# Kernel tuning notes

Hardware: AMD Instinct MI355X
Metric: run time of the kernel (lower is better)

The kernel has to match this reference:

```python
import jax, jax.numpy as jnp
import numpy as np

B, N, M = 4, 512, 8192
QUERY_DIM, INPUT_DIM = 512, 256
HEADS, DIM_HEAD = 8, 64
ATT_DIM = HEADS * DIM_HEAD  # 512


def setup_inputs() -> dict:
    key = jax.random.key(0)
    ks = jax.random.split(key, 6)
    x = jax.random.normal(ks[0], (B, N, QUERY_DIM), dtype=jnp.float32)
    context = jax.random.normal(ks[1], (B, M, INPUT_DIM), dtype=jnp.float32)
    # Linear weights stored as [in, out] for x @ W
    Wq = jax.random.normal(ks[2], (QUERY_DIM, ATT_DIM), dtype=jnp.float32) / np.sqrt(QUERY_DIM)
    Wkv = jax.random.normal(ks[3], (INPUT_DIM, 2 * ATT_DIM), dtype=jnp.float32) / np.sqrt(INPUT_DIM)
    Wo = jax.random.normal(ks[4], (ATT_DIM, QUERY_DIM), dtype=jnp.float32) / np.sqrt(ATT_DIM)
    bo = jax.random.normal(ks[5], (QUERY_DIM,), dtype=jnp.float32) * 0.01
    return {"x": x, "context": context, "Wq": Wq, "Wkv": Wkv, "Wo": Wo, "bo": bo}


def reference(x, context, Wq, Wkv, Wo, bo):
    scale = DIM_HEAD ** -0.5
    q = x @ Wq                      # [B, N, H*D]
    kv = context @ Wkv              # [B, M, 2*H*D]
    k, v = jnp.split(kv, 2, axis=-1)
    # split heads: b n (h d) -> b h n d
    q = q.reshape(B, N, HEADS, DIM_HEAD).transpose(0, 2, 1, 3)
    k = k.reshape(B, M, HEADS, DIM_HEAD).transpose(0, 2, 1, 3)
    v = v.reshape(B, M, HEADS, DIM_HEAD).transpose(0, 2, 1, 3)
    scores = jnp.einsum('bhid,bhjd->bhij', q, k) * scale  # [B, H, N, M]
    attn = jax.nn.softmax(scores, axis=-1)
    out = jnp.einsum('bhij,bhjd->bhid', attn, v)           # [B, H, N, D]
    out = out.transpose(0, 2, 1, 3).reshape(B, N, ATT_DIM)
    return out @ Wo + bo
```

## Files before the change

kernel.cpp:

```cpp
#include <hip/hip_runtime.h>
#include <hip/hip_bf16.h>
#include <cstdint>

#define NB 4
#define NQ 512
#define NM 8192
#define NH 8
#define DH 64

typedef short bf16x8s __attribute__((ext_vector_type(8)));
typedef short bf16x4s __attribute__((ext_vector_type(4)));
typedef float f32x4  __attribute__((ext_vector_type(4)));

static __device__ __forceinline__ short f2bs(float f) {
    unsigned u = __builtin_bit_cast(unsigned, f);
    return (short)(unsigned short)((u + 0x8000u) >> 16);
}
static __device__ __forceinline__ unsigned pk2(float a, float b) {
    unsigned au = __builtin_bit_cast(unsigned, a) + 0x8000u;
    unsigned bu = __builtin_bit_cast(unsigned, b) + 0x8000u;
    return __builtin_amdgcn_perm(bu, au, 0x07060302u);
}

#if __has_builtin(__builtin_amdgcn_exp2f)
static __device__ __forceinline__ float fexp2(float x) { return __builtin_amdgcn_exp2f(x); }
#else
static __device__ __forceinline__ float fexp2(float x) { return exp2f(x); }
#endif

__global__ __launch_bounds__(256) void prep_weights(
    const float* __restrict__ Wq, const float* __restrict__ Wo,
    const float* __restrict__ Wkv,
    short* __restrict__ Wqf, short* __restrict__ Wof, short* __restrict__ Wkvf)
{
    const int t = threadIdx.x;
    const int w = t >> 6, ln = t & 63;
    const int m16 = ln & 15, quad = ln >> 4;
    int f = blockIdx.x * 4 + w;
    const float* src; short* dst; int N, KS, n0, ks;
    if (f < 512)       { src = Wq;  dst = Wqf;  N = 512;  KS = 16; n0 = f >> 4; ks = f & 15; }
    else if (f < 1024) { f -= 512;  src = Wo;  dst = Wof;  N = 512;  KS = 16; n0 = f >> 4; ks = f & 15; }
    else               { f -= 1024; src = Wkv; dst = Wkvf; N = 1024; KS = 8;  n0 = f >> 3; ks = f & 7; }
    const float* sp = src + (size_t)(ks * 32 + quad * 8) * N + n0 * 16 + m16;
    float v[8];
    #pragma unroll
    for (int j = 0; j < 8; ++j) v[j] = sp[(size_t)j * N];
    uint4 pkv = { pk2(v[0],v[1]), pk2(v[2],v[3]), pk2(v[4],v[5]), pk2(v[6],v[7]) };
    *(uint4*)(dst + ((size_t)(n0 * KS + ks) * 64 + ln) * 8) = pkv;
}

__device__ __forceinline__ void proj32_body(
    const float* __restrict__ A, const short* __restrict__ Wf,
    float* __restrict__ C, const float* __restrict__ bias,
    int tm, int tn, char* smemraw)
{
    short* As = (short*)smemraw;

    const int t = threadIdx.x;
    const int w = t >> 6, ln = t & 63;
    const int m16 = ln & 15, quad = ln >> 4;
    const int wm = w >> 1, wn = w & 1;

    const int ar = t >> 3, ac = (t & 7) << 3;

    const float* Ap = A + (size_t)(tm * 32 + ar) * 512 + ac;

    f32x4 acc[2] = {};

    {
        float4 a0 = *(const float4*)(Ap);
        float4 a1 = *(const float4*)(Ap + 4);
        uint4 wa = { pk2(a0.x,a0.y), pk2(a0.z,a0.w), pk2(a1.x,a1.y), pk2(a1.z,a1.w) };
        *(uint4*)&As[ar * 72 + ac] = wa;
    }

    #pragma unroll
    for (int k0 = 0; k0 < 512; k0 += 64) {
        short* Ab = As + ((k0 >> 6) & 1) * 2304;
        __syncthreads();

        bf16x8s bfr[2][2];
        #pragma unroll
        for (int ks = 0; ks < 2; ++ks)
            #pragma unroll
            for (int nt = 0; nt < 2; ++nt)
                bfr[ks][nt] = *(const bf16x8s*)(Wf +
                    ((size_t)((tn * 4 + wn * 2 + nt) * 16 + (k0 >> 5) + ks) * 64 + ln) * 8);

        bf16x8s afr[2];
        #pragma unroll
        for (int ks = 0; ks < 2; ++ks)
            afr[ks] = *(const bf16x8s*)&Ab[(wm * 16 + m16) * 72 + ks * 32 + quad * 8];

        float4 a0n, a1n;
        if (k0 + 64 < 512) {
            a0n = *(const float4*)(Ap + k0 + 64);
            a1n = *(const float4*)(Ap + k0 + 68);
        }

        #pragma unroll
        for (int ks = 0; ks < 2; ++ks)
            #pragma unroll
            for (int nt = 0; nt < 2; ++nt)
                acc[nt] = __builtin_amdgcn_mfma_f32_16x16x32_bf16(afr[ks], bfr[ks][nt], acc[nt], 0, 0, 0);

        if (k0 + 64 < 512) {
            short* Abn = As + ((((k0 >> 6) + 1) & 1)) * 2304;
            uint4 wa = { pk2(a0n.x,a0n.y), pk2(a0n.z,a0n.w), pk2(a1n.x,a1n.y), pk2(a1n.z,a1n.w) };
            *(uint4*)&Abn[ar * 72 + ac] = wa;
        }
    }

    const int row0 = tm * 32 + wm * 16 + quad * 4;
    const int col0 = tn * 64 + wn * 32;
    #pragma unroll
    for (int nt = 0; nt < 2; ++nt) {
        const int col = col0 + nt * 16 + m16;
        const float bb = bias ? bias[col] : 0.f;
        #pragma unroll
        for (int r = 0; r < 4; ++r)
            C[(size_t)(row0 + r) * 512 + col] = acc[nt][r] + bb;
    }
}

__device__ __forceinline__ void kv_body(
    const float* __restrict__ A, const short* __restrict__ Wkvf,
    short* __restrict__ Kf, short* __restrict__ Vf,
    int kvid, char* smemraw)
{
    short* As = (short*)smemraw;

    const int t  = threadIdx.x;
    const int tm = ((kvid >> 6) << 3) | (kvid & 7);
    const int tn = (kvid >> 3) & 7;
    const int w  = t >> 6, ln = t & 63;
    const int m16 = ln & 15, quad = ln >> 4;
    const int wm = w & 1, wn = w >> 1;

    const int ar = t >> 3;
    const int ac = (t & 7) << 2;

    const float* Abase = A + (size_t)(tm * 128 + ar) * 256 + ac;

    f32x4 acc[4][4] = {};

    {
        float4 av[4];
        #pragma unroll
        for (int p = 0; p < 4; ++p)
            av[p] = *(const float4*)(Abase + (size_t)p * 32 * 256);
        #pragma unroll
        for (int p = 0; p < 4; ++p) {
            uint2 wv = { pk2(av[p].x, av[p].y), pk2(av[p].z, av[p].w) };
            *(uint2*)&As[(p * 32 + ar) * 40 + ac] = wv;
        }
    }

    #pragma unroll
    for (int k0 = 0; k0 < 256; k0 += 32) {
        short* Ab = As + ((k0 >> 5) & 1) * 5120;
        __syncthreads();

        bf16x8s bfr[4];
        #pragma unroll
        for (int j = 0; j < 4; ++j)
            bfr[j] = *(const bf16x8s*)(Wkvf +
                ((size_t)((tn * 8 + wn * 4 + j) * 8 + (k0 >> 5)) * 64 + ln) * 8);

        bf16x8s af[4];
        #pragma unroll
        for (int i = 0; i < 4; ++i)
            af[i] = *(const bf16x8s*)&Ab[(wm * 64 + i * 16 + m16) * 40 + quad * 8];

        float4 avn[4];
        if (k0 + 32 < 256) {
            #pragma unroll
            for (int p = 0; p < 4; ++p)
                avn[p] = *(const float4*)(Abase + (size_t)p * 32 * 256 + k0 + 32);
        }

        #pragma unroll
        for (int i = 0; i < 4; ++i)
            #pragma unroll
            for (int j = 0; j < 4; ++j)
                acc[i][j] = __builtin_amdgcn_mfma_f32_16x16x32_bf16(af[i], bfr[j], acc[i][j], 0, 0, 0);

        if (k0 + 32 < 256) {
            short* Abn = As + (((k0 >> 5) + 1) & 1) * 5120;
            #pragma unroll
            for (int p = 0; p < 4; ++p) {
                uint2 wv = { pk2(avn[p].x, avn[p].y), pk2(avn[p].z, avn[p].w) };
                *(uint2*)&Abn[(p * 32 + ar) * 40 + ac] = wv;
            }
        }
    }

    const int col0 = tn * 128 + wn * 64;
    const int row0 = tm * 128 + wm * 64;
    const int b    = row0 >> 13;
    const int mr0  = row0 & (NM - 1);

    if (col0 < 512) {
        const int h = col0 >> 6;
        short* Kp = Kf + (size_t)(b * NH + h) * (NM * DH);
        #pragma unroll
        for (int i = 0; i < 4; ++i)
            #pragma unroll
            for (int j = 0; j < 4; ++j) {
                const int d = j * 16 + m16;
                #pragma unroll
                for (int r = 0; r < 4; ++r) {
                    const int key = mr0 + i * 16 + quad * 4 + r;
                    const int idx = ((key >> 4) * 2 + (d >> 5)) * 512
                                  + (((d >> 3) & 3) * 16 + (key & 15)) * 8 + (d & 7);
                    Kp[idx] = f2bs(acc[i][j][r]);
                }
            }
    } else {
        const int h = (col0 - 512) >> 6;
        short* Vp = Vf + (size_t)(b * NH + h) * (NM * DH);
        #pragma unroll
        for (int j = 0; j < 4; ++j)
            #pragma unroll
            for (int p = 0; p < 2; ++p) {
                uint4 v;
                v.x = pk2(acc[2*p    ][j][0], acc[2*p    ][j][1]);
                v.y = pk2(acc[2*p    ][j][2], acc[2*p    ][j][3]);
                v.z = pk2(acc[2*p + 1][j][0], acc[2*p + 1][j][1]);
                v.w = pk2(acc[2*p + 1][j][2], acc[2*p + 1][j][3]);
                *(uint4*)(Vp + ((size_t)(j * 256 + (mr0 >> 5) + p) * 64 + ln) * 8) = v;
            }
    }
}

__global__ __launch_bounds__(256) void gemm_kvq(
    const float* __restrict__ x,   const short* __restrict__ Wqf, float* __restrict__ q,
    const float* __restrict__ ctx, const short* __restrict__ Wkvf,
    short* __restrict__ Kf, short* __restrict__ Vf)
{
    __shared__ __align__(16) char smem[20480];
    if (blockIdx.x < 512)
        proj32_body(x, Wqf, q, nullptr, (int)(blockIdx.x >> 3), (int)(blockIdx.x & 7), smem);
    else
        kv_body(ctx, Wkvf, Kf, Vf, (int)(blockIdx.x - 512), smem);
}

__global__ __launch_bounds__(256) void gemm_proj32(
    const float* __restrict__ A, const short* __restrict__ Wf,
    float* __restrict__ C, const float* __restrict__ bias)
{
    __shared__ __align__(16) char smem[32 * 72 * 2 * 2];
    proj32_body(A, Wf, C, bias, (int)(blockIdx.x >> 3), (int)(blockIdx.x & 7), smem);
}

__global__ __launch_bounds__(512, 2) void attn_mfma(
    const float* __restrict__ Q,
    const short* __restrict__ Kfr,
    const short* __restrict__ Vfr,
    float* __restrict__ Og)
{
    __shared__ __align__(16) float Ob[2][64 * 66];
    __shared__ float lbuf[8 * 64];

    const int bid = blockIdx.x;
    const int xcd = bid & 7, g = bid >> 3;
    const int bh  = xcd * 4 + (g & 3);
    const int qt  = g >> 2;
    const int b   = bh >> 3, h = bh & 7;
    const int t   = threadIdx.x;
    const int w   = t >> 6, ln = t & 63;
    const int m16 = ln & 15, quad = ln >> 4;

    const short* Kbase = Kfr + (size_t)bh * (NM * DH);
    const short* Vbase = Vfr + (size_t)bh * (NM * DH);

    const float qsc = 0.125f * 1.44269504f;
    bf16x8s qf[4][2];
    #pragma unroll
    for (int mt = 0; mt < 4; ++mt) {
        const float* qrow = Q + ((size_t)(b * NQ + qt * 64 + mt * 16 + m16)) * 512 + h * 64;
        #pragma unroll
        for (int ks = 0; ks < 2; ++ks) {
            float4 x0 = *(const float4*)(qrow + ks * 32 + quad * 8);
            float4 x1 = *(const float4*)(qrow + ks * 32 + quad * 8 + 4);
            uint4 pkv = { pk2(x0.x * qsc, x0.y * qsc), pk2(x0.z * qsc, x0.w * qsc),
                          pk2(x1.x * qsc, x1.y * qsc), pk2(x1.z * qsc, x1.w * qsc) };
            qf[mt][ks] = *reinterpret_cast<bf16x8s*>(&pkv);
        }
    }

    bf16x4s ones4;
    #pragma unroll
    for (int j = 0; j < 4; ++j) ones4[j] = (short)0x3F80;

    f32x4 o[4][4] = {};
    f32x4 lsum[4] = {};

    bf16x8s kf[4][2];
    {
        const int kc = w * 64;
        #pragma unroll
        for (int nt = 0; nt < 4; ++nt)
            #pragma unroll
            for (int ks = 0; ks < 2; ++ks)
                kf[nt][ks] = *(const bf16x8s*)(Kbase + ((((kc >> 4) + nt) * 2 + ks) << 9) + ln * 8);
    }

    for (int it = 0; it < 16; ++it) {
        const int kc = it * 512 + w * 64;

        uint4 vraw[4][2];
        #pragma unroll
        for (int dt = 0; dt < 4; ++dt)
            #pragma unroll
            for (int kp = 0; kp < 2; ++kp)
                vraw[dt][kp] = *(const uint4*)(Vbase + ((size_t)(dt * 256 + (kc >> 5) + kp) * 64 + ln) * 8);

        f32x4 st[4][4] = {};
        #pragma unroll
        for (int kt = 0; kt < 4; ++kt)
            #pragma unroll
            for (int mt = 0; mt < 4; ++mt) {
                st[mt][kt] = __builtin_amdgcn_mfma_f32_16x16x32_bf16(kf[kt][0], qf[mt][0], st[mt][kt], 0, 0, 0);
                st[mt][kt] = __builtin_amdgcn_mfma_f32_16x16x32_bf16(kf[kt][1], qf[mt][1], st[mt][kt], 0, 0, 0);
            }

        if (it + 1 < 16) {
            const int kn = (it + 1) * 512 + w * 64;
            #pragma unroll
            for (int nt = 0; nt < 4; ++nt)
                #pragma unroll
                for (int ks = 0; ks < 2; ++ks)
                    kf[nt][ks] = *(const bf16x8s*)(Kbase + ((((kn >> 4) + nt) * 2 + ks) << 9) + ln * 8);
        }

        #pragma unroll
        for (int mt = 0; mt < 4; ++mt)
            #pragma unroll
            for (int kt = 0; kt < 4; ++kt) {
                const float p0 = fexp2(st[mt][kt][0]);
                const float p1 = fexp2(st[mt][kt][1]);
                const float p2 = fexp2(st[mt][kt][2]);
                const float p3 = fexp2(st[mt][kt][3]);
                uint2 pu = { pk2(p0, p1), pk2(p2, p3) };
                bf16x4s pbv = *reinterpret_cast<bf16x4s*>(&pu);
                const int kp = kt >> 1, hh = kt & 1;
                #pragma unroll
                for (int dt = 0; dt < 4; ++dt) {
                    uint2 vh = hh ? make_uint2(vraw[dt][kp].z, vraw[dt][kp].w)
                                  : make_uint2(vraw[dt][kp].x, vraw[dt][kp].y);
                    bf16x4s va = *reinterpret_cast<bf16x4s*>(&vh);
                    o[mt][dt] = __builtin_amdgcn_mfma_f32_16x16x16bf16_1k(va, pbv, o[mt][dt], 0, 0, 0);
                }
                lsum[mt] = __builtin_amdgcn_mfma_f32_16x16x16bf16_1k(ones4, pbv, lsum[mt], 0, 0, 0);
            }
    }

    if (quad == 0) {
        #pragma unroll
        for (int mt = 0; mt < 4; ++mt)
            lbuf[w * 64 + mt * 16 + m16] = lsum[mt][0];
    }
    if (w < 2) {
        float* dst = Ob[w];
        #pragma unroll
        for (int mt = 0; mt < 4; ++mt)
            #pragma unroll
            for (int dt = 0; dt < 4; ++dt)
                *(f32x4*)&dst[(mt * 16 + m16) * 66 + dt * 16 + quad * 4] = o[mt][dt];
    }
    __syncthreads();
    #pragma unroll
    for (int ph = 1; ph < 4; ++ph) {
        if ((w >> 1) == ph) {
            float* dst = Ob[w & 1];
            #pragma unroll
            for (int mt = 0; mt < 4; ++mt)
                #pragma unroll
                for (int dt = 0; dt < 4; ++dt) {
                    float* p = &dst[(mt * 16 + m16) * 66 + dt * 16 + quad * 4];
                    f32x4 cur = *(f32x4*)p;
                    cur += o[mt][dt];
                    *(f32x4*)p = cur;
                }
        }
        __syncthreads();
    }
    {
        const int row = t >> 3;
        const int d0  = (t & 7) << 3;
        float l = 0.f;
        #pragma unroll
        for (int wi = 0; wi < 8; ++wi) l += lbuf[wi * 64 + row];
        const float inv = 1.0f / l;
        float* op = Og + ((size_t)(b * NQ + qt * 64 + row)) * 512 + h * 64 + d0;
        #pragma unroll
        for (int j = 0; j < 2; ++j) {
            const int c = row * 66 + d0 + j * 4;
            float4 r;
            r.x = (Ob[0][c + 0] + Ob[1][c + 0]) * inv;
            r.y = (Ob[0][c + 1] + Ob[1][c + 1]) * inv;
            r.z = (Ob[0][c + 2] + Ob[1][c + 2]) * inv;
            r.w = (Ob[0][c + 3] + Ob[1][c + 3]) * inv;
            *(float4*)(op + j * 4) = r;
        }
    }
}

extern "C" void kernel_launch(void* const* d_in, const int* in_sizes, int n_in,
                              void* d_out, int out_size, void* d_ws, size_t ws_size,
                              hipStream_t stream) {
    (void)in_sizes; (void)n_in; (void)out_size; (void)ws_size;

    const float* x   = (const float*)d_in[0];
    const float* ctx = (const float*)d_in[1];
    const float* Wq  = (const float*)d_in[2];
    const float* Wkv = (const float*)d_in[3];
    const float* Wo  = (const float*)d_in[4];
    const float* bo  = (const float*)d_in[5];
    float* out = (float*)d_out;

    float* ws    = (float*)d_ws;
    float* q     = ws;
    float* attno = q + (size_t)2048 * 512;
    short* Kf    = (short*)(attno + (size_t)2048 * 512);
    short* Vf    = Kf + (size_t)NB * NH * NM * DH;
    short* Wqf   = Vf + (size_t)NB * NH * NM * DH;
    short* Wof   = Wqf + (size_t)512 * 512;
    short* Wkvf  = Wof + (size_t)512 * 512;

    prep_weights<<<dim3(384), dim3(256), 0, stream>>>(Wq, Wo, Wkv, Wqf, Wof, Wkvf);

    gemm_kvq<<<dim3(2560), dim3(256), 0, stream>>>(x, Wqf, q, ctx, Wkvf, Kf, Vf);

    attn_mfma<<<dim3(256), dim3(512), 0, stream>>>(q, Kf, Vf, attno);

    gemm_proj32<<<dim3(512), dim3(256), 0, stream>>>(attno, Wof, out, bo);
}
```

Baseline: 187.5 us.

## Split attention over key halves, merge in output projection, restructure KV GEMM

Attention now splits the key range into two halves per block (512 blocks instead of 256), writing unnormalized partial outputs and row sums. The output projection adds the two partials and normalizes them before the bf16 GEMM. The KV projection uses 512-thread blocks covering 256 output columns, stages weights through double-buffered LDS, and writes K via an LDS transpose for coalesced stores. MFMA sections get s_setprio hints. The aim is higher occupancy and parallelism, at the cost of an extra partial buffer and more LDS per block.

```diff
diff --git a/kernel.cpp b/kernel.cpp
--- a/kernel.cpp
+++ b/kernel.cpp
@@ -52,11 +52,10 @@
 __device__ __forceinline__ void proj32_body(
     const float* __restrict__ A, const short* __restrict__ Wf,
     float* __restrict__ C, const float* __restrict__ bias,
-    int tm, int tn, char* smemraw)
+    int tm, int tn, char* smemraw, int t)
 {
     short* As = (short*)smemraw;
 
-    const int t = threadIdx.x;
     const int w = t >> 6, ln = t & 63;
     const int m16 = ln & 15, quad = ln >> 4;
     const int wm = w >> 1, wn = w & 1;
@@ -123,99 +122,203 @@
     }
 }
 
+__device__ __forceinline__ void projo_body(
+    const float* __restrict__ A0, const float* __restrict__ A1,
+    const float* __restrict__ l0p, const float* __restrict__ l1p,
+    const short* __restrict__ Wf,
+    float* __restrict__ C, const float* __restrict__ bias,
+    int tm, int tn, char* smemraw, int t)
+{
+    short* As = (short*)smemraw;
+
+    const int w = t >> 6, ln = t & 63;
+    const int m16 = ln & 15, quad = ln >> 4;
+    const int wm = w >> 1, wn = w & 1;
+
+    const int ar = t >> 3, ac = (t & 7) << 3;
+
+    const int row = tm * 32 + ar;
+    const int lbase = ((row >> 9) * NH) * NQ + (row & 511);
+
+    float sc[8];
+    #pragma unroll
+    for (int h = 0; h < 8; ++h)
+        sc[h] = 1.0f / (l0p[lbase + h * NQ] + l1p[lbase + h * NQ]);
+
+    const float* Ap0 = A0 + (size_t)row * 512 + ac;
+    const float* Ap1 = A1 + (size_t)row * 512 + ac;
+
+    f32x4 acc[2] = {};
+
+    {
+        float4 a0 = *(const float4*)(Ap0);
+        float4 b0 = *(const float4*)(Ap1);
+        float4 a1 = *(const float4*)(Ap0 + 4);
+        float4 b1 = *(const float4*)(Ap1 + 4);
+        const float s = sc[0];
+        uint4 wa = { pk2((a0.x+b0.x)*s,(a0.y+b0.y)*s), pk2((a0.z+b0.z)*s,(a0.w+b0.w)*s),
+                     pk2((a1.x+b1.x)*s,(a1.y+b1.y)*s), pk2((a1.z+b1.z)*s,(a1.w+b1.w)*s) };
+        *(uint4*)&As[ar * 72 + ac] = wa;
+    }
+
+    #pragma unroll
+    for (int k0 = 0; k0 < 512; k0 += 64) {
+        short* Ab = As + ((k0 >> 6) & 1) * 2304;
+        __syncthreads();
+
+        bf16x8s bfr[2][2];
+        #pragma unroll
+        for (int ks = 0; ks < 2; ++ks)
+            #pragma unroll
+            for (int nt = 0; nt < 2; ++nt)
+                bfr[ks][nt] = *(const bf16x8s*)(Wf +
+                    ((size_t)((tn * 4 + wn * 2 + nt) * 16 + (k0 >> 5) + ks) * 64 + ln) * 8);
+
+        bf16x8s afr[2];
+        #pragma unroll
+        for (int ks = 0; ks < 2; ++ks)
+            afr[ks] = *(const bf16x8s*)&Ab[(wm * 16 + m16) * 72 + ks * 32 + quad * 8];
+
+        float4 a0n, b0n, a1n, b1n;
+        if (k0 + 64 < 512) {
+            a0n = *(const float4*)(Ap0 + k0 + 64);
+            b0n = *(const float4*)(Ap1 + k0 + 64);
+            a1n = *(const float4*)(Ap0 + k0 + 68);
+            b1n = *(const float4*)(Ap1 + k0 + 68);
+        }
+
+        #pragma unroll
+        for (int ks = 0; ks < 2; ++ks)
+            #pragma unroll
+            for (int nt = 0; nt < 2; ++nt)
+                acc[nt] = __builtin_amdgcn_mfma_f32_16x16x32_bf16(afr[ks], bfr[ks][nt], acc[nt], 0, 0, 0);
+
+        if (k0 + 64 < 512) {
+            short* Abn = As + ((((k0 >> 6) + 1) & 1)) * 2304;
+            const float s = sc[(k0 >> 6) + 1];
+            uint4 wa = { pk2((a0n.x+b0n.x)*s,(a0n.y+b0n.y)*s), pk2((a0n.z+b0n.z)*s,(a0n.w+b0n.w)*s),
+                         pk2((a1n.x+b1n.x)*s,(a1n.y+b1n.y)*s), pk2((a1n.z+b1n.z)*s,(a1n.w+b1n.w)*s) };
+            *(uint4*)&Abn[ar * 72 + ac] = wa;
+        }
+    }
+
+    const int row0 = tm * 32 + wm * 16 + quad * 4;
+    const int col0 = tn * 64 + wn * 32;
+    #pragma unroll
+    for (int nt = 0; nt < 2; ++nt) {
+        const int col = col0 + nt * 16 + m16;
+        const float bb = bias[col];
+        #pragma unroll
+        for (int r = 0; r < 4; ++r)
+            C[(size_t)(row0 + r) * 512 + col] = acc[nt][r] + bb;
+    }
+}
+
 __device__ __forceinline__ void kv_body(
     const float* __restrict__ A, const short* __restrict__ Wkvf,
     short* __restrict__ Kf, short* __restrict__ Vf,
     int kvid, char* smemraw)
 {
     short* As = (short*)smemraw;
+    short* Ws = (short*)(smemraw + 20480);
 
     const int t  = threadIdx.x;
-    const int tm = ((kvid >> 6) << 3) | (kvid & 7);
-    const int tn = (kvid >> 3) & 7;
+    const int tm  = ((kvid >> 5) << 3) | (kvid & 7);
+    const int tn0 = (kvid >> 3) & 3;
     const int w  = t >> 6, ln = t & 63;
     const int m16 = ln & 15, quad = ln >> 4;
     const int wm = w & 1, wn = w >> 1;
 
-    const int ar = t >> 3;
-    const int ac = (t & 7) << 2;
-
-    const float* Abase = A + (size_t)(tm * 128 + ar) * 256 + ac;
+    const int ar  = t >> 2;
+    const int acf = (t & 3) << 3;
+
+    const float* Abase = A + (size_t)(tm * 128 + ar) * 256 + acf;
+    const short* Wb = Wkvf + (size_t)tn0 * 16 * 8 * 512;
 
     f32x4 acc[4][4] = {};
 
     {
-        float4 av[4];
-        #pragma unroll
-        for (int p = 0; p < 4; ++p)
-            av[p] = *(const float4*)(Abase + (size_t)p * 32 * 256);
-        #pragma unroll
-        for (int p = 0; p < 4; ++p) {
-            uint2 wv = { pk2(av[p].x, av[p].y), pk2(av[p].z, av[p].w) };
-            *(uint2*)&As[(p * 32 + ar) * 40 + ac] = wv;
-        }
-    }
-
-    #pragma unroll
-    for (int k0 = 0; k0 < 256; k0 += 32) {
-        short* Ab = As + ((k0 >> 5) & 1) * 5120;
+        float4 a0 = *(const float4*)(Abase);
+        float4 a1 = *(const float4*)(Abase + 4);
+        uint4 wa = { pk2(a0.x,a0.y), pk2(a0.z,a0.w), pk2(a1.x,a1.y), pk2(a1.z,a1.w) };
+        *(uint4*)&As[ar * 40 + acf] = wa;
+        uint4 w0 = *(const uint4*)(Wb + ((size_t)(w * 8)) * 512 + ln * 8);
+        uint4 w1 = *(const uint4*)(Wb + ((size_t)((8 + w) * 8)) * 512 + ln * 8);
+        *(uint4*)&Ws[w * 512 + ln * 8] = w0;
+        *(uint4*)&Ws[4096 + w * 512 + ln * 8] = w1;
+    }
+
+    #pragma unroll
+    for (int s = 0; s < 8; ++s) {
+        const int b = s & 1;
+        short* Ab = As + b * 5120;
+        short* Wc = Ws + b * 8192;
         __syncthreads();
 
+        uint4 w0n, w1n; float4 a0n, a1n;
+        if (s < 7) {
+            w0n = *(const uint4*)(Wb + ((size_t)(w * 8) + (s + 1)) * 512 + ln * 8);
+            w1n = *(const uint4*)(Wb + ((size_t)((8 + w) * 8) + (s + 1)) * 512 + ln * 8);
+            a0n = *(const float4*)(Abase + (s + 1) * 32);
+            a1n = *(const float4*)(Abase + (s + 1) * 32 + 4);
+        }
+
         bf16x8s bfr[4];
         #pragma unroll
         for (int j = 0; j < 4; ++j)
-            bfr[j] = *(const bf16x8s*)(Wkvf +
-                ((size_t)((tn * 8 + wn * 4 + j) * 8 + (k0 >> 5)) * 64 + ln) * 8);
-
+            bfr[j] = *(const bf16x8s*)&Wc[(wn * 4 + j) * 512 + ln * 8];
         bf16x8s af[4];
         #pragma unroll
         for (int i = 0; i < 4; ++i)
             af[i] = *(const bf16x8s*)&Ab[(wm * 64 + i * 16 + m16) * 40 + quad * 8];
 
-        float4 avn[4];
-        if (k0 + 32 < 256) {
-            #pragma unroll
-            for (int p = 0; p < 4; ++p)
-                avn[p] = *(const float4*)(Abase + (size_t)p * 32 * 256 + k0 + 32);
-        }
-
         #pragma unroll
         for (int i = 0; i < 4; ++i)
             #pragma unroll
             for (int j = 0; j < 4; ++j)
                 acc[i][j] = __builtin_amdgcn_mfma_f32_16x16x32_bf16(af[i], bfr[j], acc[i][j], 0, 0, 0);
 
-        if (k0 + 32 < 256) {
-            short* Abn = As + (((k0 >> 5) + 1) & 1) * 5120;
-            #pragma unroll
-            for (int p = 0; p < 4; ++p) {
-                uint2 wv = { pk2(avn[p].x, avn[p].y), pk2(avn[p].z, avn[p].w) };
-                *(uint2*)&Abn[(p * 32 + ar) * 40 + ac] = wv;
-            }
-        }
-    }
-
-    const int col0 = tn * 128 + wn * 64;
+        if (s < 7) {
+            short* Abn = As + (b ^ 1) * 5120;
+            short* Wcn = Ws + (b ^ 1) * 8192;
+            uint4 wa = { pk2(a0n.x,a0n.y), pk2(a0n.z,a0n.w), pk2(a1n.x,a1n.y), pk2(a1n.z,a1n.w) };
+            *(uint4*)&Abn[ar * 40 + acf] = wa;
+            *(uint4*)&Wcn[w * 512 + ln * 8] = w0n;
+            *(uint4*)&Wcn[4096 + w * 512 + ln * 8] = w1n;
+        }
+    }
+
+    const int col0 = tn0 * 256 + wn * 64;
     const int row0 = tm * 128 + wm * 64;
     const int b    = row0 >> 13;
     const int mr0  = row0 & (NM - 1);
 
     if (col0 < 512) {
+        __syncthreads();
         const int h = col0 >> 6;
         short* Kp = Kf + (size_t)(b * NH + h) * (NM * DH);
-        #pragma unroll
-        for (int i = 0; i < 4; ++i)
-            #pragma unroll
-            for (int j = 0; j < 4; ++j) {
-                const int d = j * 16 + m16;
+        short* S  = (short*)smemraw + w * 2048;
+        #pragma unroll
+        for (int half = 0; half < 2; ++half) {
+            const int i0 = half * 2;
+            #pragma unroll
+            for (int di = 0; di < 2; ++di)
                 #pragma unroll
-                for (int r = 0; r < 4; ++r) {
-                    const int key = mr0 + i * 16 + quad * 4 + r;
-                    const int idx = ((key >> 4) * 2 + (d >> 5)) * 512
-                                  + (((d >> 3) & 3) * 16 + (key & 15)) * 8 + (d & 7);
-                    Kp[idx] = f2bs(acc[i][j][r]);
+                for (int j = 0; j < 4; ++j) {
+                    const int d    = j * 16 + m16;
+                    const int fl   = di * 2 + (d >> 5);
+                    const int base = fl * 512 + (((d >> 3) & 3) * 16 + quad * 4) * 8 + (d & 7);
+                    #pragma unroll
+                    for (int r = 0; r < 4; ++r)
+                        S[base + r * 8] = f2bs(acc[i0 + di][j][r]);
                 }
+            const int gf0 = ((mr0 >> 4) + i0) * 2;
+            #pragma unroll
+            for (int fl = 0; fl < 4; ++fl) {
+                uint4 v = *(const uint4*)&S[fl * 512 + ln * 8];
+                *(uint4*)(Kp + ((size_t)(gf0 + fl) * 512 + ln * 8)) = v;
             }
+        }
     } else {
         const int h = (col0 - 512) >> 6;
         short* Vp = Vf + (size_t)(b * NH + h) * (NM * DH);
@@ -233,31 +336,38 @@
     }
 }
 
-__global__ __launch_bounds__(256) void gemm_kvq(
+__global__ __launch_bounds__(512, 4) void gemm_kvq(
     const float* __restrict__ x,   const short* __restrict__ Wqf, float* __restrict__ q,
     const float* __restrict__ ctx, const short* __restrict__ Wkvf,
     short* __restrict__ Kf, short* __restrict__ Vf)
 {
-    __shared__ __align__(16) char smem[20480];
-    if (blockIdx.x < 512)
-        proj32_body(x, Wqf, q, nullptr, (int)(blockIdx.x >> 3), (int)(blockIdx.x & 7), smem);
-    else
-        kv_body(ctx, Wkvf, Kf, Vf, (int)(blockIdx.x - 512), smem);
+    __shared__ __align__(16) char smem[53248];
+    if (blockIdx.x < 256) {
+        const int u = (int)(blockIdx.x * 2) + (int)(threadIdx.x >> 8);
+        proj32_body(x, Wqf, q, nullptr, u >> 3, u & 7,
+                    smem + (threadIdx.x >> 8) * 9216, (int)(threadIdx.x & 255));
+    } else {
+        kv_body(ctx, Wkvf, Kf, Vf, (int)(blockIdx.x - 256), smem);
+    }
 }
 
 __global__ __launch_bounds__(256) void gemm_proj32(
-    const float* __restrict__ A, const short* __restrict__ Wf,
+    const float* __restrict__ A0, const float* __restrict__ A1,
+    const float* __restrict__ l0, const float* __restrict__ l1,
+    const short* __restrict__ Wf,
     float* __restrict__ C, const float* __restrict__ bias)
 {
     __shared__ __align__(16) char smem[32 * 72 * 2 * 2];
-    proj32_body(A, Wf, C, bias, (int)(blockIdx.x >> 3), (int)(blockIdx.x & 7), smem);
-}
-
-__global__ __launch_bounds__(512, 2) void attn_mfma(
+    projo_body(A0, A1, l0, l1, Wf, C, bias,
+               (int)(blockIdx.x >> 3), (int)(blockIdx.x & 7), smem, (int)threadIdx.x);
+}
+
+__global__ __launch_bounds__(512, 4) void attn_mfma(
     const float* __restrict__ Q,
     const short* __restrict__ Kfr,
     const short* __restrict__ Vfr,
-    float* __restrict__ Og)
+    float* __restrict__ Op,
+    float* __restrict__ Lp)
 {
     __shared__ __align__(16) float Ob[2][64 * 66];
     __shared__ float lbuf[8 * 64];
@@ -265,7 +375,8 @@
     const int bid = blockIdx.x;
     const int xcd = bid & 7, g = bid >> 3;
     const int bh  = xcd * 4 + (g & 3);
-    const int qt  = g >> 2;
+    const int qt  = (g >> 2) & 7;
+    const int kh  = g >> 5;
     const int b   = bh >> 3, h = bh & 7;
     const int t   = threadIdx.x;
     const int w   = t >> 6, ln = t & 63;
@@ -273,6 +384,7 @@
 
     const short* Kbase = Kfr + (size_t)bh * (NM * DH);
     const short* Vbase = Vfr + (size_t)bh * (NM * DH);
+    const int it0 = kh * 8;
 
     const float qsc = 0.125f * 1.44269504f;
     bf16x8s qf[4][2];
@@ -298,7 +410,7 @@
 
     bf16x8s kf[4][2];
     {
-        const int kc = w * 64;
+        const int kc = it0 * 512 + w * 64;
         #pragma unroll
         for (int nt = 0; nt < 4; ++nt)
             #pragma unroll
@@ -306,7 +418,7 @@
                 kf[nt][ks] = *(const bf16x8s*)(Kbase + ((((kc >> 4) + nt) * 2 + ks) << 9) + ln * 8);
     }
 
-    for (int it = 0; it < 16; ++it) {
+    for (int it = it0; it < it0 + 8; ++it) {
         const int kc = it * 512 + w * 64;
 
         uint4 vraw[4][2];
@@ -317,6 +429,7 @@
                 vraw[dt][kp] = *(const uint4*)(Vbase + ((size_t)(dt * 256 + (kc >> 5) + kp) * 64 + ln) * 8);
 
         f32x4 st[4][4] = {};
+        __builtin_amdgcn_s_setprio(1);
         #pragma unroll
         for (int kt = 0; kt < 4; ++kt)
             #pragma unroll
@@ -324,8 +437,9 @@
                 st[mt][kt] = __builtin_amdgcn_mfma_f32_16x16x32_bf16(kf[kt][0], qf[mt][0], st[mt][kt], 0, 0, 0);
                 st[mt][kt] = __builtin_amdgcn_mfma_f32_16x16x32_bf16(kf[kt][1], qf[mt][1], st[mt][kt], 0, 0, 0);
             }
-
-        if (it + 1 < 16) {
+        __builtin_amdgcn_s_setprio(0);
+
+        if (it + 1 < it0 + 8) {
             const int kn = (it + 1) * 512 + w * 64;
             #pragma unroll
             for (int nt = 0; nt < 4; ++nt)
@@ -345,6 +459,7 @@
                 uint2 pu = { pk2(p0, p1), pk2(p2, p3) };
                 bf16x4s pbv = *reinterpret_cast<bf16x4s*>(&pu);
                 const int kp = kt >> 1, hh = kt & 1;
+                __builtin_amdgcn_s_setprio(1);
                 #pragma unroll
                 for (int dt = 0; dt < 4; ++dt) {
                     uint2 vh = hh ? make_uint2(vraw[dt][kp].z, vraw[dt][kp].w)
@@ -353,6 +468,7 @@
                     o[mt][dt] = __builtin_amdgcn_mfma_f32_16x16x16bf16_1k(va, pbv, o[mt][dt], 0, 0, 0);
                 }
                 lsum[mt] = __builtin_amdgcn_mfma_f32_16x16x16bf16_1k(ones4, pbv, lsum[mt], 0, 0, 0);
+                __builtin_amdgcn_s_setprio(0);
             }
     }
 
@@ -387,22 +503,25 @@
         __syncthreads();
     }
     {
+        float* Og = Op + (size_t)kh * (2048 * 512);
         const int row = t >> 3;
         const int d0  = (t & 7) << 3;
-        float l = 0.f;
-        #pragma unroll
-        for (int wi = 0; wi < 8; ++wi) l += lbuf[wi * 64 + row];
-        const float inv = 1.0f / l;
         float* op = Og + ((size_t)(b * NQ + qt * 64 + row)) * 512 + h * 64 + d0;
         #pragma unroll
         for (int j = 0; j < 2; ++j) {
             const int c = row * 66 + d0 + j * 4;
             float4 r;
-            r.x = (Ob[0][c + 0] + Ob[1][c + 0]) * inv;
-            r.y = (Ob[0][c + 1] + Ob[1][c + 1]) * inv;
-            r.z = (Ob[0][c + 2] + Ob[1][c + 2]) * inv;
-            r.w = (Ob[0][c + 3] + Ob[1][c + 3]) * inv;
+            r.x = Ob[0][c + 0] + Ob[1][c + 0];
+            r.y = Ob[0][c + 1] + Ob[1][c + 1];
+            r.z = Ob[0][c + 2] + Ob[1][c + 2];
+            r.w = Ob[0][c + 3] + Ob[1][c + 3];
             *(float4*)(op + j * 4) = r;
+        }
+        if (t < 64) {
+            float l = 0.f;
+            #pragma unroll
+            for (int wi = 0; wi < 8; ++wi) l += lbuf[wi * 64 + t];
+            Lp[(size_t)kh * (32 * NQ) + bh * NQ + qt * 64 + t] = l;
         }
     }
 }
@@ -423,7 +542,8 @@
     float* ws    = (float*)d_ws;
     float* q     = ws;
     float* attno = q + (size_t)2048 * 512;
-    short* Kf    = (short*)(attno + (size_t)2048 * 512);
+    float* lws   = attno + (size_t)2 * 2048 * 512;
+    short* Kf    = (short*)(lws + (size_t)2 * 32 * NQ);
     short* Vf    = Kf + (size_t)NB * NH * NM * DH;
     short* Wqf   = Vf + (size_t)NB * NH * NM * DH;
     short* Wof   = Wqf + (size_t)512 * 512;
@@ -431,9 +551,11 @@
 
     prep_weights<<<dim3(384), dim3(256), 0, stream>>>(Wq, Wo, Wkv, Wqf, Wof, Wkvf);
 
-    gemm_kvq<<<dim3(2560), dim3(256), 0, stream>>>(x, Wqf, q, ctx, Wkvf, Kf, Vf);
-
-    attn_mfma<<<dim3(256), dim3(512), 0, stream>>>(q, Kf, Vf, attno);
-
-    gemm_proj32<<<dim3(512), dim3(256), 0, stream>>>(attno, Wof, out, bo);
-}
+    gemm_kvq<<<dim3(1280), dim3(512), 0, stream>>>(x, Wqf, q, ctx, Wkvf, Kf, Vf);
+
+    attn_mfma<<<dim3(512), dim3(512), 0, stream>>>(q, Kf, Vf, attno, lws);
+
+    gemm_proj32<<<dim3(512), dim3(256), 0, stream>>>(
+        attno, attno + (size_t)2048 * 512, lws, lws + (size_t)32 * NQ,
+        Wof, out, bo);
+}
```

Result: slower. 548.9 us (+192.7%).
